# Performance work log

Hardware: AMD Instinct MI355X
Metric: run time of the kernel (lower is better)

Reference implementation:

```python
import jax, jax.numpy as jnp
import numpy as np


def _margins(labels):
    # labels: [B, L] int. Imposter index j = roll(i+1, wrap).
    lab_j = jnp.roll(labels, -1, axis=0)
    equal = jnp.all(labels == lab_j, axis=1)                 # [B]
    n = jnp.sum(labels | lab_j, axis=1).astype(jnp.float32)  # union count
    diff = jnp.sum(labels ^ lab_j, axis=1).astype(jnp.float32)
    margin = jnp.maximum(0.5, diff / jnp.maximum(n, 1.0))
    return jnp.where(equal, 0.0, margin)                     # [B]


def setup_inputs() -> dict:
    key = jax.random.key(0)
    k1, k2, k3 = jax.random.split(key, 3)
    B, D, L = 16384, 512, 14
    z_image = jax.random.normal(k1, (B, D), dtype=jnp.float32)
    z_text = jax.random.normal(k2, (B, D), dtype=jnp.float32)
    labels = jax.random.randint(k3, (B, L), 0, 2, dtype=jnp.int32)
    return {"z_image": z_image, "z_text": z_text, "labels": labels}


def reference(z_image, z_text, labels):
    # similarity_function='dot' (default in forward call sites)
    B = z_image.shape[0]
    margin = _margins(labels)                                 # [B]
    paired = jnp.sum(z_image * z_text, axis=1)                # [B] dot(z_image[i], z_text[i])
    zi_j = jnp.roll(z_image, -1, axis=0)                      # z_image[j]
    zt_j = jnp.roll(z_text, -1, axis=0)                       # z_text[j]
    imp_img = jnp.sum(zi_j * z_text, axis=1)                  # dot(z_image[j], z_text[i])
    imp_txt = jnp.sum(zt_j * z_image, axis=1)                 # dot(z_text[j], z_image[i])
    loss_img = jnp.sum(jnp.maximum(imp_img - paired + margin, 0.0)) / B
    loss_txt = jnp.sum(jnp.maximum(imp_txt - paired + margin, 0.0)) / B
    return (loss_img + loss_txt).reshape(1)
```

## Files before the change

### kernel.cpp

```cpp
#include <hip/hip_runtime.h>


constexpr int B = 16384;
constexpr int D = 512;
constexpr int L = 14;
constexpr int BLOCK = 256;
constexpr int WPB = BLOCK / 64;
constexpr int R = 8;
constexpr int GRID = B / (WPB * R);

__device__ __forceinline__ float dot4(float4 a, float4 b) {
    return a.x * b.x + a.y * b.y + a.z * b.z + a.w * b.w;
}

__global__ __launch_bounds__(BLOCK) void rank_main(
    const float* __restrict__ zi, const float* __restrict__ zt,
    const int* __restrict__ labels, float* __restrict__ ws)
{
    const int lane = threadIdx.x & 63;
    const int wv   = threadIdx.x >> 6;
    const int gw   = blockIdx.x * WPB + wv;
    const int base = gw * R;

    const float4* zi4 = (const float4*)zi;
    const float4* zt4 = (const float4*)zt;

    size_t o = (size_t)base * 128 + lane;
    float4 a0 = zi4[o], a1 = zi4[o + 64];
    float4 b0 = zt4[o], b1 = zt4[o + 64];
    int lab = (lane < L) ? labels[base * L + lane] : 0;
    float pd = dot4(a0, b0) + dot4(a1, b1);

    float acc = 0.0f;

    #pragma unroll
    for (int r = 0; r < R; ++r) {
        const int nrow = (base + r + 1) & (B - 1);
        const size_t no = (size_t)nrow * 128 + lane;
        const float4 na0 = zi4[no], na1 = zi4[no + 64];
        const float4 nb0 = zt4[no], nb1 = zt4[no + 64];
        const int nlab = (lane < L) ? labels[nrow * L + lane] : 0;

        float pii = dot4(na0, b0) + dot4(na1, b1);
        float pit = dot4(nb0, a0) + dot4(nb1, a1);
        float npd = dot4(na0, nb0) + dot4(na1, nb1);

        const unsigned long long bor  = __ballot((lab | nlab) != 0);
        const unsigned long long bxor = __ballot((lab ^ nlab) != 0);

        float s0 = pd, s1 = pii, s2 = pit;
        #pragma unroll
        for (int off = 32; off > 0; off >>= 1) {
            s0 += __shfl_down(s0, off);
            s1 += __shfl_down(s1, off);
            s2 += __shfl_down(s2, off);
        }

        if (lane == 0) {
            const int df = __popcll(bxor);
            float margin = 0.0f;
            if (df != 0) {
                const int n = __popcll(bor);
                margin = fmaxf(0.5f, (float)df / (float)n);
            }
            acc += fmaxf(s1 - s0 + margin, 0.0f)
                 + fmaxf(s2 - s0 + margin, 0.0f);
        }

        a0 = na0; a1 = na1; b0 = nb0; b1 = nb1;
        lab = nlab; pd = npd;
    }

    __shared__ float s[WPB];
    if (lane == 0) s[wv] = acc;
    __syncthreads();
    if (threadIdx.x == 0)
        ws[blockIdx.x] = s[0] + s[1] + s[2] + s[3];
}

__global__ __launch_bounds__(BLOCK) void rank_reduce(
    const float* __restrict__ ws, float* __restrict__ out)
{
    float v = ws[threadIdx.x] + ws[threadIdx.x + BLOCK];
    #pragma unroll
    for (int off = 32; off > 0; off >>= 1) v += __shfl_down(v, off);
    __shared__ float s[WPB];
    if ((threadIdx.x & 63) == 0) s[threadIdx.x >> 6] = v;
    __syncthreads();
    if (threadIdx.x == 0)
        out[0] = (s[0] + s[1] + s[2] + s[3]) * (1.0f / (float)B);
}

extern "C" void kernel_launch(void* const* d_in, const int* in_sizes, int n_in,
                              void* d_out, int out_size, void* d_ws, size_t ws_size,
                              hipStream_t stream) {
    const float* zi     = (const float*)d_in[0];
    const float* zt     = (const float*)d_in[1];
    const int*   labels = (const int*)d_in[2];
    float* out = (float*)d_out;
    float* ws  = (float*)d_ws;

    rank_main<<<GRID, BLOCK, 0, stream>>>(zi, zt, labels, ws);
    rank_reduce<<<1, BLOCK, 0, stream>>>(ws, out);
}
```

Before: 99.23 us.

## Split each row strip across two waves, halving per-wave loads

```diff
diff --git a/kernel.cpp b/kernel.cpp
--- a/kernel.cpp
+++ b/kernel.cpp
@@ -2,12 +2,11 @@
 
 
 constexpr int B = 16384;
-constexpr int D = 512;
 constexpr int L = 14;
 constexpr int BLOCK = 256;
-constexpr int WPB = BLOCK / 64;
 constexpr int R = 8;
-constexpr int GRID = B / (WPB * R);
+constexpr int STRIPS_PER_BLOCK = 2;
+constexpr int GRID = B / (STRIPS_PER_BLOCK * R);
 
 __device__ __forceinline__ float dot4(float4 a, float4 b) {
     return a.x * b.x + a.y * b.y + a.z * b.z + a.w * b.w;
@@ -19,75 +18,90 @@
 {
     const int lane = threadIdx.x & 63;
     const int wv   = threadIdx.x >> 6;
-    const int gw   = blockIdx.x * WPB + wv;
-    const int base = gw * R;
+    const int pair = wv >> 1;
+    const int half = wv & 1;
+    const int base = (blockIdx.x * STRIPS_PER_BLOCK + pair) * R;
 
     const float4* zi4 = (const float4*)zi;
     const float4* zt4 = (const float4*)zt;
 
-    size_t o = (size_t)base * 128 + lane;
-    float4 a0 = zi4[o], a1 = zi4[o + 64];
-    float4 b0 = zt4[o], b1 = zt4[o + 64];
-    int lab = (lane < L) ? labels[base * L + lane] : 0;
-    float pd = dot4(a0, b0) + dot4(a1, b1);
+    __shared__ float sdot[4][R][3];
+    __shared__ float smar[STRIPS_PER_BLOCK][R];
 
-    float acc = 0.0f;
+    size_t o = (size_t)base * 128 + half * 64 + lane;
+    float4 a = zi4[o];
+    float4 b = zt4[o];
+    int lab = (half == 0 && lane < L) ? labels[base * L + lane] : 0;
+    float pd = dot4(a, b);
 
     #pragma unroll
     for (int r = 0; r < R; ++r) {
         const int nrow = (base + r + 1) & (B - 1);
-        const size_t no = (size_t)nrow * 128 + lane;
-        const float4 na0 = zi4[no], na1 = zi4[no + 64];
-        const float4 nb0 = zt4[no], nb1 = zt4[no + 64];
-        const int nlab = (lane < L) ? labels[nrow * L + lane] : 0;
+        const size_t no = (size_t)nrow * 128 + half * 64 + lane;
+        const float4 na = zi4[no];
+        const float4 nb = zt4[no];
+        const int nlab = (half == 0 && lane < L) ? labels[nrow * L + lane] : 0;
 
-        float pii = dot4(na0, b0) + dot4(na1, b1);
-        float pit = dot4(nb0, a0) + dot4(nb1, a1);
-        float npd = dot4(na0, nb0) + dot4(na1, nb1);
+        float s0 = pd;
+        float s1 = dot4(na, b);
+        float s2 = dot4(nb, a);
+        const float npd = dot4(na, nb);
 
-        const unsigned long long bor  = __ballot((lab | nlab) != 0);
-        const unsigned long long bxor = __ballot((lab ^ nlab) != 0);
+        if (half == 0) {
+            const unsigned long long bor  = __ballot((lab | nlab) != 0);
+            const unsigned long long bxor = __ballot((lab ^ nlab) != 0);
+            if (lane == 0) {
+                const int df = __popcll(bxor);
+                float margin = 0.0f;
+                if (df != 0)
+                    margin = fmaxf(0.5f, (float)df / (float)__popcll(bor));
+                smar[pair][r] = margin;
+            }
+        }
 
-        float s0 = pd, s1 = pii, s2 = pit;
         #pragma unroll
         for (int off = 32; off > 0; off >>= 1) {
             s0 += __shfl_down(s0, off);
             s1 += __shfl_down(s1, off);
             s2 += __shfl_down(s2, off);
         }
-
         if (lane == 0) {
-            const int df = __popcll(bxor);
-            float margin = 0.0f;
-            if (df != 0) {
-                const int n = __popcll(bor);
-                margin = fmaxf(0.5f, (float)df / (float)n);
-            }
-            acc += fmaxf(s1 - s0 + margin, 0.0f)
-                 + fmaxf(s2 - s0 + margin, 0.0f);
+            sdot[wv][r][0] = s0;
+            sdot[wv][r][1] = s1;
+            sdot[wv][r][2] = s2;
         }
 
-        a0 = na0; a1 = na1; b0 = nb0; b1 = nb1;
-        lab = nlab; pd = npd;
+        a = na; b = nb; lab = nlab; pd = npd;
     }
 
-    __shared__ float s[WPB];
-    if (lane == 0) s[wv] = acc;
     __syncthreads();
-    if (threadIdx.x == 0)
-        ws[blockIdx.x] = s[0] + s[1] + s[2] + s[3];
+
+    const int t = threadIdx.x;
+    float hinge = 0.0f;
+    if (t < STRIPS_PER_BLOCK * R) {
+        const int p = t >> 3, r = t & 7;
+        const float q0 = sdot[p * 2][r][0] + sdot[p * 2 + 1][r][0];
+        const float q1 = sdot[p * 2][r][1] + sdot[p * 2 + 1][r][1];
+        const float q2 = sdot[p * 2][r][2] + sdot[p * 2 + 1][r][2];
+        const float m  = smar[p][r];
+        hinge = fmaxf(q1 - q0 + m, 0.0f) + fmaxf(q2 - q0 + m, 0.0f);
+    }
+    #pragma unroll
+    for (int off = 8; off > 0; off >>= 1) hinge += __shfl_down(hinge, off);
+    if (t == 0) ws[blockIdx.x] = hinge;
 }
 
 __global__ __launch_bounds__(BLOCK) void rank_reduce(
     const float* __restrict__ ws, float* __restrict__ out)
 {
-    float v = ws[threadIdx.x] + ws[threadIdx.x + BLOCK];
+    const int t = threadIdx.x;
+    float v = ws[t] + ws[t + 256] + ws[t + 512] + ws[t + 768];
     #pragma unroll
     for (int off = 32; off > 0; off >>= 1) v += __shfl_down(v, off);
-    __shared__ float s[WPB];
-    if ((threadIdx.x & 63) == 0) s[threadIdx.x >> 6] = v;
+    __shared__ float s[4];
+    if ((t & 63) == 0) s[t >> 6] = v;
     __syncthreads();
-    if (threadIdx.x == 0)
+    if (t == 0)
         out[0] = (s[0] + s[1] + s[2] + s[3]) * (1.0f / (float)B);
 }
 
```

Result: no change. 99.57 us (+0.3%).
